# Kernel optimization log

Hardware: AMD Instinct MI355X
Metric: run time of the kernel (lower is better)

## Reference

```python
import jax, jax.numpy as jnp
import numpy as np
import math

E = 8          # num_exp
K = 2          # top-k
IN_D = 1024
HD = 2048
BS = 8
SEQ = 2048
CAP_FACTOR = 1.25
MIN_CAP = 4


def setup_inputs() -> dict:
    key = jax.random.key(0)
    ks = jax.random.split(key, 5)
    s = 0.02  # init scale for weights
    x = jax.random.normal(ks[0], (BS, SEQ, IN_D), jnp.float32)
    gate_w = jax.random.normal(ks[1], (E, IN_D), jnp.float32) * s
    fc1_w = jax.random.normal(ks[2], (E, HD, IN_D), jnp.float32) * s
    gating_w = jax.random.normal(ks[3], (E, HD, IN_D), jnp.float32) * s
    fc2_w = jax.random.normal(ks[4], (E, IN_D, HD), jnp.float32) * s
    return {"x": x, "gate_w": gate_w, "fc1_w": fc1_w, "gating_w": gating_w, "fc2_w": fc2_w}


def reference(x, gate_w, fc1_w, gating_w, fc2_w):
    bs, seq, d = x.shape
    N = bs * seq
    NK = N * K
    # capacity in slots per expert (static given shapes)
    capacity = max(int(math.ceil(((NK + E - 1) // E) * CAP_FACTOR)), MIN_CAP)
    dummy = E * capacity  # overflow slot index

    # --- routing ---
    logits = jnp.einsum('bsd,ed->bse', x, gate_w)
    probs = jax.nn.softmax(logits.astype(jnp.float32), axis=-1)
    # load-balancing probs use detached x
    logits_lbl = jnp.einsum('bsd,ed->bse', jax.lax.stop_gradient(x), gate_w)
    probs_lbl = jax.nn.softmax(logits_lbl.astype(jnp.float32), axis=-1)

    topk_vals, topk_inds = jax.lax.top_k(probs, K)          # [bs,seq,K]
    cl = topk_vals / (topk_vals.sum(-1, keepdims=True) + 1e-9)

    x_exp = jnp.repeat(x.reshape(N, d), K, axis=0)          # [NK, d]
    exp_ids = topk_inds.reshape(NK)
    w_flat = cl.reshape(NK).astype(x.dtype)

    # --- dispatch: stable sort by expert id ---
    sort_perm = jnp.argsort(exp_ids * NK + jnp.arange(NK))
    sorted_exp = exp_ids[sort_perm]
    sorted_x = x_exp[sort_perm]
    sorted_w = w_flat[sort_perm]

    counts = jnp.zeros((E,), jnp.int32).at[sorted_exp].add(1)
    starts = jnp.cumsum(counts) - counts
    local_pos = jnp.arange(NK) - starts[sorted_exp]
    keep = local_pos < capacity
    slot = jnp.where(keep, sorted_exp * capacity + local_pos, dummy)

    buf = jnp.zeros((dummy + 1, d), x.dtype).at[slot].set(sorted_x)
    buf_x = buf[:-1].reshape(E, capacity, d)

    # --- per-expert SwiGLU FFN as grouped matmuls ---
    h = jax.nn.silu(jnp.einsum('ecd,ehd->ech', buf_x, fc1_w)) * \
        jnp.einsum('ecd,ehd->ech', buf_x, gating_w)
    buf_out = jnp.einsum('ech,edh->ecd', h, fc2_w)           # [E,cap,d]

    # --- combine ---
    buf_full = jnp.concatenate([buf_out.reshape(dummy, d),
                                jnp.zeros((1, d), x.dtype)], axis=0)
    w_masked = sorted_w * keep.astype(sorted_w.dtype)
    out_sorted = buf_full[slot] * w_masked[:, None]
    out_dispatch = jnp.zeros((NK, d), x.dtype).at[sort_perm].set(out_sorted)
    moe_out = out_dispatch.reshape(N, K, d).sum(axis=1).reshape(bs, seq, d)

    # --- balancing loss ---
    p = probs_lbl.mean(axis=(0, 1))
    f = jax.lax.stop_gradient(
        jnp.zeros((E,), jnp.float32).at[exp_ids].add(1.0) / NK)
    balancing_loss = E * jnp.sum(p * f)
    return moe_out.astype(x.dtype), balancing_loss
```

## Files before the change

kernel.cpp:

```cpp
#include <hip/hip_runtime.h>

#define E_NUM 8
#define DIM   1024
#define HDIM  2048
#define N_TOK 16384
#define NKA   32768
#define CAP   5120
#define REG_SZ 16777216

typedef __bf16 bf16x8 __attribute__((ext_vector_type(8)));
typedef float  f32x4  __attribute__((ext_vector_type(4)));

__device__ __forceinline__ unsigned short f2b(float f) {
  union { float f; unsigned u; } v; v.f = f;
  unsigned r = (v.u + 0x7FFFu + ((v.u >> 16) & 1u)) >> 16;
  return (unsigned short)r;
}

__device__ __forceinline__ void gload16(const void* g, void* l) {
  __builtin_amdgcn_global_load_lds(
      (const __attribute__((address_space(1))) unsigned int*)g,
      (__attribute__((address_space(3))) unsigned int*)l, 16, 0, 0);
}

template<int N> __device__ __forceinline__ void wait_vmcnt() {
  if constexpr (N == 10)      asm volatile("s_waitcnt vmcnt(10)" ::: "memory");
  else if constexpr (N == 8)  asm volatile("s_waitcnt vmcnt(8)"  ::: "memory");
  else if constexpr (N == 4)  asm volatile("s_waitcnt vmcnt(4)"  ::: "memory");
  else if constexpr (N == 2)  asm volatile("s_waitcnt vmcnt(2)"  ::: "memory");
  else if constexpr (N == 0)  asm volatile("s_waitcnt vmcnt(0)"  ::: "memory");
}

__global__ __launch_bounds__(256) void cast_kernel(
    const float* __restrict__ s0, const float* __restrict__ s1,
    const float* __restrict__ s2, const float* __restrict__ s3,
    unsigned short* __restrict__ dst) {
  int region = blockIdx.y;
  const float* src = region == 0 ? s0 : region == 1 ? s1 : region == 2 ? s2 : s3;
  size_t i = ((size_t)blockIdx.x * 256 + threadIdx.x) * 8;
  float4 v0 = *(const float4*)(src + i);
  float4 v1 = *(const float4*)(src + i + 4);
  ushort4 u0 = { f2b(v0.x), f2b(v0.y), f2b(v0.z), f2b(v0.w) };
  ushort4 u1 = { f2b(v1.x), f2b(v1.y), f2b(v1.z), f2b(v1.w) };
  unsigned short* o = dst + (size_t)region * REG_SZ + i;
  *(ushort4*)o = u0;
  *(ushort4*)(o + 4) = u1;
}

__global__ __launch_bounds__(256) void routing_kernel(
    const float* __restrict__ x, const float* __restrict__ gate_w,
    int* __restrict__ cnt, float* __restrict__ p_sum,
    int* __restrict__ tok_of_slot, float* __restrict__ w_of_slot) {
  __shared__ float p_acc[E_NUM];
  __shared__ int   lcnt[E_NUM];
  __shared__ int   l_tok[E_NUM][128];
  __shared__ float l_w[E_NUM][128];
  __shared__ int   base[E_NUM];

  int t = threadIdx.x, lane = t & 63, wave = t >> 6;
  if (t < E_NUM) { p_acc[t] = 0.f; lcnt[t] = 0; }
  __syncthreads();

  for (int it = 0; it < 16; ++it) {
    int token = blockIdx.x * 64 + it * 4 + wave;
    const float4* xr = (const float4*)(x + (size_t)token * DIM);
    float4 xv[4];
    #pragma unroll
    for (int i = 0; i < 4; ++i) xv[i] = xr[lane + 64 * i];
    float s[E_NUM];
    #pragma unroll
    for (int e = 0; e < E_NUM; ++e) {
      const float4* gr = (const float4*)(gate_w + e * DIM);
      float acc = 0.f;
      #pragma unroll
      for (int i = 0; i < 4; ++i) {
        float4 g = gr[lane + 64 * i];
        acc += xv[i].x * g.x + xv[i].y * g.y + xv[i].z * g.z + xv[i].w * g.w;
      }
      s[e] = acc;
    }
    #pragma unroll
    for (int e = 0; e < E_NUM; ++e) {
      float v = s[e];
      #pragma unroll
      for (int off = 32; off; off >>= 1) v += __shfl_down(v, off);
      s[e] = v;
    }
    if (lane == 0) {
      float m = s[0];
      #pragma unroll
      for (int e = 1; e < E_NUM; ++e) m = fmaxf(m, s[e]);
      float p[E_NUM]; float sum = 0.f;
      #pragma unroll
      for (int e = 0; e < E_NUM; ++e) { p[e] = expf(s[e] - m); sum += p[e]; }
      float inv = 1.f / sum;
      #pragma unroll
      for (int e = 0; e < E_NUM; ++e) p[e] *= inv;
      int e0 = 0; float v0 = p[0];
      #pragma unroll
      for (int e = 1; e < E_NUM; ++e) if (p[e] > v0) { v0 = p[e]; e0 = e; }
      int e1 = -1; float v1 = -1.f;
      #pragma unroll
      for (int e = 0; e < E_NUM; ++e) if (e != e0 && p[e] > v1) { v1 = p[e]; e1 = e; }
      float denom = v0 + v1 + 1e-9f;
      float w0 = v0 / denom, w1 = v1 / denom;
      #pragma unroll
      for (int e = 0; e < E_NUM; ++e) atomicAdd(&p_acc[e], p[e]);
      int i0 = atomicAdd(&lcnt[e0], 1); l_tok[e0][i0] = token; l_w[e0][i0] = w0;
      int i1 = atomicAdd(&lcnt[e1], 1); l_tok[e1][i1] = token; l_w[e1][i1] = w1;
    }
  }
  __syncthreads();
  if (t < E_NUM) {
    base[t] = atomicAdd(&cnt[t], lcnt[t]);
    atomicAdd(&p_sum[t], p_acc[t]);
  }
  __syncthreads();
  int e = t >> 5, i0 = t & 31;
  int n = lcnt[e], b = base[e];
  for (int i = i0; i < n; i += 32) {
    int pos = b + i;
    if (pos < CAP) {
      tok_of_slot[e * CAP + pos] = l_tok[e][i];
      w_of_slot[e * CAP + pos]   = l_w[e][i];
    }
  }
}

__global__ void loss_kernel(const int* __restrict__ cnt,
                            const float* __restrict__ p_sum,
                            float* __restrict__ out_loss) {
  if (threadIdx.x == 0) {
    float acc = 0.f;
    for (int e = 0; e < E_NUM; ++e)
      acc += (p_sum[e] / (float)N_TOK) * ((float)cnt[e] / (float)NKA);
    *out_loss = (float)E_NUM * acc;
  }
}


__device__ __forceinline__ void lda_f(const unsigned short* Ab, bf16x8 af[2][4],
                                      int rowbase, const int cs[2]) {
  const unsigned short* base = Ab + rowbase * 64;
  #pragma unroll
  for (int mt = 0; mt < 4; ++mt) {
    af[0][mt] = *(const bf16x8*)&base[mt * 1024 + cs[0]];
    af[1][mt] = *(const bf16x8*)&base[mt * 1024 + cs[1]];
  }
}
__device__ __forceinline__ void ldb_f(const unsigned short* Bb, bf16x8 bf[2][2],
                                      int rowbase, const int cs[2]) {
  const unsigned short* base = Bb + rowbase * 64;
  #pragma unroll
  for (int nt = 0; nt < 2; ++nt) {
    bf[0][nt] = *(const bf16x8*)&base[nt * 1024 + cs[0]];
    bf[1][nt] = *(const bf16x8*)&base[nt * 1024 + cs[1]];
  }
}

template<int MH, int NH>
__device__ __forceinline__ void mmq(f32x4 acc[8][4], const bf16x8 af[2][4],
                                    const bf16x8 bf[2][2]) {
  #pragma unroll
  for (int mt = 0; mt < 4; ++mt)
    #pragma unroll
    for (int nt = 0; nt < 2; ++nt) {
      f32x4 c = acc[MH * 4 + mt][NH * 2 + nt];
      c = __builtin_amdgcn_mfma_f32_16x16x32_bf16(af[0][mt], bf[0][nt], c, 0, 0, 0);
      c = __builtin_amdgcn_mfma_f32_16x16x32_bf16(af[1][mt], bf[1][nt], c, 0, 0, 0);
      acc[MH * 4 + mt][NH * 2 + nt] = c;
    }
}

#define A_LDS(b) (&LDS[(b) * 16384])
#define B_LDS(b) (&LDS[32768 + (b) * 16384])

#define STAGE_A(b, h, kk) { \
  gload16(srcA[h][0] + (kk) * 64, &LDS[(b) * 16384 + (h) * 8192 + wave * 512]); \
  gload16(srcA[h][1] + (kk) * 64, &LDS[(b) * 16384 + (h) * 8192 + 4096 + wave * 512]); }
#define STAGE_B(b, h, kk) { \
  gload16(srcB[h][0] + (kk) * 64, &LDS[32768 + (b) * 16384 + (h) * 8192 + wave * 512]); \
  gload16(srcB[h][1] + (kk) * 64, &LDS[32768 + (b) * 16384 + (h) * 8192 + 4096 + wave * 512]); }

#define MIDBAR \
  __builtin_amdgcn_s_barrier(); \
  asm volatile("s_waitcnt lgkmcnt(0)" ::: "memory"); \
  __builtin_amdgcn_sched_barrier(0); \
  __builtin_amdgcn_s_setprio(1);

#define ENDBAR(W) \
  __builtin_amdgcn_s_setprio(0); \
  wait_vmcnt<W>(); \
  __builtin_amdgcn_s_barrier();

#define TILE_BODY(W1T, W2T, W4T, S1, S2) { \
  const int cur = kt & 1, oth = cur ^ 1; \
  lda_f(A_LDS(cur), af, g64r, cs); \
  ldb_f(B_LDS(cur), bfA, q32r, cs); \
  if (S1) STAGE_A(oth, 1, kt + 1); \
  MIDBAR; mmq<0, 0>(acc, af, bfA); ENDBAR(W1T); \
  ldb_f(B_LDS(cur), bfB, 128 + q32r, cs); \
  if (S2) STAGE_A(cur, 0, kt + 2); \
  MIDBAR; mmq<0, 1>(acc, af, bfB); ENDBAR(W2T); \
  lda_f(A_LDS(cur), af, 128 + g64r, cs); \
  if (S2) STAGE_B(cur, 0, kt + 2); \
  MIDBAR; mmq<1, 1>(acc, af, bfB); ENDBAR(-1); \
  if (S2) STAGE_B(cur, 1, kt + 2); \
  MIDBAR; mmq<1, 0>(acc, af, bfA); ENDBAR(W4T); \
}

#define GEMM_PROLOGUE { \
  STAGE_A(0, 0, 0); STAGE_B(0, 0, 0); STAGE_B(0, 1, 0); STAGE_A(0, 1, 0); \
  STAGE_A(1, 0, 1); STAGE_B(1, 0, 1); STAGE_B(1, 1, 1); \
  wait_vmcnt<10>(); \
  __builtin_amdgcn_s_barrier(); }

#define GEMM_MAIN(NTK) \
  GEMM_PROLOGUE; \
  for (int kt = 0; kt < (NTK) - 2; ++kt) TILE_BODY(10, 10, 10, true, true); \
  { int kt = (NTK) - 2; TILE_BODY(10, 8, 4, true, false); } \
  { int kt = (NTK) - 1; TILE_BODY(2, 0, -1, false, false); }

__global__ __launch_bounds__(512, 2) void gemm1_kernel(
    const unsigned short* __restrict__ Wb,
    const int* __restrict__ cnt, const int* __restrict__ tok_of_slot,
    unsigned short* __restrict__ Hbuf, int e_base) {
  int ez = blockIdx.z, e = e_base + ez;
  int cntc = min(cnt[e], CAP);
  int m0 = blockIdx.y * 256;
  if (m0 >= cntc) return;
  int n0 = blockIdx.x * 256;

  __shared__ __align__(16) unsigned short LDS[65536];

  int tid = threadIdx.x;
  int wave = tid >> 6, lane = tid & 63;
  int quad = lane >> 4, r = lane & 15;
  int gm = (wave >> 2) * 64, qn = (wave & 3) * 32;
  int g64r = gm + r, q32r = qn + r;
  int cs[2] = { (quad ^ (r & 7)) * 8, ((4 + quad) ^ (r & 7)) * 8 };

  const unsigned short* W1e = Wb + (size_t)e * HDIM * DIM;
  const unsigned short* Wge = Wb + REG_SZ + (size_t)e * HDIM * DIM;
  const unsigned short* Xb  = Wb + (size_t)3 * REG_SZ;

  const unsigned short* srcA[2][2];
  const unsigned short* srcB[2][2];
  #pragma unroll
  for (int j = 0; j < 2; ++j) {
    int row = (j * 512 + tid) >> 3;
    int co  = ((tid & 7) ^ (row & 7)) * 8;
    #pragma unroll
    for (int h = 0; h < 2; ++h) {
      int slot = m0 + h * 128 + row;
      int tok = (slot < cntc) ? tok_of_slot[e * CAP + slot] : 0;
      srcA[h][j] = Xb + (size_t)tok * DIM + co;
      int nglob = n0 + h * 128 + row;
      const unsigned short* wsrc = (nglob & 1) ? Wge : W1e;
      srcB[h][j] = wsrc + (size_t)(nglob >> 1) * DIM + co;
    }
  }

  f32x4 acc[8][4];
  #pragma unroll
  for (int i = 0; i < 8; ++i)
    #pragma unroll
    for (int jj = 0; jj < 4; ++jj) acc[i][jj] = (f32x4)0.f;
  bf16x8 af[2][4], bfA[2][2], bfB[2][2];

  GEMM_MAIN(16);

  #pragma unroll
  for (int mh = 0; mh < 2; ++mh)
    #pragma unroll
    for (int mt = 0; mt < 4; ++mt)
      #pragma unroll
      for (int reg = 0; reg < 4; ++reg) {
        int row = m0 + mh * 128 + gm + mt * 16 + quad * 4 + reg;
        bool wr = (row < cntc);
        size_t basei = (size_t)(ez * CAP + row) * HDIM;
        #pragma unroll
        for (int nh = 0; nh < 2; ++nh)
          #pragma unroll
          for (int nt = 0; nt < 2; ++nt) {
            float v = acc[mh * 4 + mt][nh * 2 + nt][reg];
            float o = __shfl_xor(v, 1);
            if (wr && !(lane & 1)) {
              float a = v, b = o;
              float hval = (a / (1.f + __expf(-a))) * b;
              int coln = n0 + nh * 128 + qn + nt * 16 + r;
              Hbuf[basei + (coln >> 1)] = f2b(hval);
            }
          }
      }
}

__global__ __launch_bounds__(512, 2) void gemm2_kernel(
    const unsigned short* __restrict__ Hbuf, const unsigned short* __restrict__ Wb,
    const int* __restrict__ cnt, const int* __restrict__ tok_of_slot,
    const float* __restrict__ w_of_slot, float* __restrict__ out, int e_base) {
  int ez = blockIdx.z, e = e_base + ez;
  int cntc = min(cnt[e], CAP);
  int m0 = blockIdx.y * 256;
  if (m0 >= cntc) return;
  int n0 = blockIdx.x * 256;

  __shared__ __align__(16) unsigned short LDS[65536];

  int tid = threadIdx.x;
  int wave = tid >> 6, lane = tid & 63;
  int quad = lane >> 4, r = lane & 15;
  int gm = (wave >> 2) * 64, qn = (wave & 3) * 32;
  int g64r = gm + r, q32r = qn + r;
  int cs[2] = { (quad ^ (r & 7)) * 8, ((4 + quad) ^ (r & 7)) * 8 };

  const unsigned short* W2e = Wb + (size_t)2 * REG_SZ + (size_t)e * DIM * HDIM;
  const unsigned short* He  = Hbuf + (size_t)(ez * CAP) * HDIM;

  const unsigned short* srcA[2][2];
  const unsigned short* srcB[2][2];
  #pragma unroll
  for (int j = 0; j < 2; ++j) {
    int row = (j * 512 + tid) >> 3;
    int co  = ((tid & 7) ^ (row & 7)) * 8;
    #pragma unroll
    for (int h = 0; h < 2; ++h) {
      srcA[h][j] = He + (size_t)(m0 + h * 128 + row) * HDIM + co;
      srcB[h][j] = W2e + (size_t)(n0 + h * 128 + row) * HDIM + co;
    }
  }

  f32x4 acc[8][4];
  #pragma unroll
  for (int i = 0; i < 8; ++i)
    #pragma unroll
    for (int jj = 0; jj < 4; ++jj) acc[i][jj] = (f32x4)0.f;
  bf16x8 af[2][4], bfA[2][2], bfB[2][2];

  GEMM_MAIN(32);

  #pragma unroll
  for (int mh = 0; mh < 2; ++mh)
    #pragma unroll
    for (int mt = 0; mt < 4; ++mt)
      #pragma unroll
      for (int reg = 0; reg < 4; ++reg) {
        int rowl = m0 + mh * 128 + gm + mt * 16 + quad * 4 + reg;
        if (rowl >= cntc) continue;
        int tok = tok_of_slot[e * CAP + rowl];
        float w = w_of_slot[e * CAP + rowl];
        float* orow = out + (size_t)tok * DIM + n0;
        #pragma unroll
        for (int nh = 0; nh < 2; ++nh)
          #pragma unroll
          for (int nt = 0; nt < 2; ++nt)
            atomicAdd(&orow[nh * 128 + qn + nt * 16 + r],
                      acc[mh * 4 + mt][nh * 2 + nt][reg] * w);
      }
}

extern "C" void kernel_launch(void* const* d_in, const int* in_sizes, int n_in,
                              void* d_out, int out_size, void* d_ws, size_t ws_size,
                              hipStream_t stream) {
  const float* x        = (const float*)d_in[0];
  const float* gate_w   = (const float*)d_in[1];
  const float* fc1_w    = (const float*)d_in[2];
  const float* gating_w = (const float*)d_in[3];
  const float* fc2_w    = (const float*)d_in[4];
  float* out = (float*)d_out;

  char* ws = (char*)d_ws;
  int*   cnt         = (int*)ws;
  float* p_sum       = (float*)(ws + 128);
  int*   tok_of_slot = (int*)(ws + 256);
  float* w_of_slot   = (float*)(ws + 256 + 163840);
  unsigned short* Wb   = (unsigned short*)(ws + 256 + 2 * 163840);
  size_t hbuf_off = 256 + 2 * 163840 + (size_t)4 * REG_SZ * 2;
  unsigned short* Hbuf = (unsigned short*)(ws + hbuf_off);

  const size_t per_e = (size_t)CAP * HDIM * 2;
  int chunkE = 1;
  if (ws_size > hbuf_off + per_e) {
    size_t c = (ws_size - hbuf_off) / per_e;
    chunkE = c >= 8 ? 8 : (int)c;
  }

  hipMemsetAsync(ws, 0, 256, stream);
  hipMemsetAsync(d_out, 0, (size_t)out_size * sizeof(float), stream);

  cast_kernel<<<dim3(8192, 4), 256, 0, stream>>>(fc1_w, gating_w, fc2_w, x, Wb);
  routing_kernel<<<256, 256, 0, stream>>>(x, gate_w, cnt, p_sum, tok_of_slot, w_of_slot);
  loss_kernel<<<1, 64, 0, stream>>>(cnt, p_sum, out + (size_t)N_TOK * DIM);

  for (int eb = 0; eb < E_NUM; eb += chunkE) {
    int ne = (E_NUM - eb) < chunkE ? (E_NUM - eb) : chunkE;
    gemm1_kernel<<<dim3(16, 20, ne), 512, 0, stream>>>(Wb, cnt, tok_of_slot, Hbuf, eb);
    gemm2_kernel<<<dim3(4, 20, ne), 512, 0, stream>>>(Hbuf, Wb, cnt, tok_of_slot, w_of_slot, out, eb);
  }
}
```

Baseline: 943.5 us.

## Replace atomic scatter with bf16 expert output buffer and gather-combine kernel

gemm2 no longer scatters its results into the fp32 output with atomicAdd. It writes bf16 per-slot rows into reused workspace regions (the dead fc1/gating weight copies and the x copy). A new combine kernel then gathers each token's two slots, weights them and writes the output, so the output memset and the atomic traffic go away. The x-to-bf16 cast is folded into the routing kernel, and blocks are remapped so that each XCD handles a single expert, which should improve L2 weight reuse. The cost is an extra bf16 rounding of the expert outputs and an extra kernel pass.

```diff
diff --git a/kernel.cpp b/kernel.cpp
--- a/kernel.cpp
+++ b/kernel.cpp
@@ -15,6 +15,11 @@
   union { float f; unsigned u; } v; v.f = f;
   unsigned r = (v.u + 0x7FFFu + ((v.u >> 16) & 1u)) >> 16;
   return (unsigned short)r;
+}
+
+__device__ __forceinline__ size_t obuf_off(int e) {
+  return (e < 6) ? (size_t)e * ((size_t)CAP * DIM)
+                 : (size_t)3 * REG_SZ + (size_t)(e - 6) * ((size_t)CAP * DIM);
 }
 
 __device__ __forceinline__ void gload16(const void* g, void* l) {
@@ -50,7 +55,9 @@
 __global__ __launch_bounds__(256) void routing_kernel(
     const float* __restrict__ x, const float* __restrict__ gate_w,
     int* __restrict__ cnt, float* __restrict__ p_sum,
-    int* __restrict__ tok_of_slot, float* __restrict__ w_of_slot) {
+    int* __restrict__ tok_of_slot, float* __restrict__ w_of_slot,
+    int* __restrict__ slot_of_tok, float* __restrict__ w_of_tok,
+    unsigned short* __restrict__ xb_out) {
   __shared__ float p_acc[E_NUM];
   __shared__ int   lcnt[E_NUM];
   __shared__ int   l_tok[E_NUM][128];
@@ -67,6 +74,12 @@
     float4 xv[4];
     #pragma unroll
     for (int i = 0; i < 4; ++i) xv[i] = xr[lane + 64 * i];
+    unsigned short* xo = xb_out + (size_t)token * DIM;
+    #pragma unroll
+    for (int i = 0; i < 4; ++i) {
+      ushort4 u = { f2b(xv[i].x), f2b(xv[i].y), f2b(xv[i].z), f2b(xv[i].w) };
+      *(ushort4*)(xo + 4 * (lane + 64 * i)) = u;
+    }
     float s[E_NUM];
     #pragma unroll
     for (int e = 0; e < E_NUM; ++e) {
@@ -106,8 +119,8 @@
       float w0 = v0 / denom, w1 = v1 / denom;
       #pragma unroll
       for (int e = 0; e < E_NUM; ++e) atomicAdd(&p_acc[e], p[e]);
-      int i0 = atomicAdd(&lcnt[e0], 1); l_tok[e0][i0] = token; l_w[e0][i0] = w0;
-      int i1 = atomicAdd(&lcnt[e1], 1); l_tok[e1][i1] = token; l_w[e1][i1] = w1;
+      int i0 = atomicAdd(&lcnt[e0], 1); l_tok[e0][i0] = (token << 1);     l_w[e0][i0] = w0;
+      int i1 = atomicAdd(&lcnt[e1], 1); l_tok[e1][i1] = (token << 1) | 1; l_w[e1][i1] = w1;
     }
   }
   __syncthreads();
@@ -121,8 +134,13 @@
   for (int i = i0; i < n; i += 32) {
     int pos = b + i;
     if (pos < CAP) {
-      tok_of_slot[e * CAP + pos] = l_tok[e][i];
-      w_of_slot[e * CAP + pos]   = l_w[e][i];
+      int tk = l_tok[e][i];
+      int token = tk >> 1, kb = tk & 1;
+      int slot = e * CAP + pos;
+      tok_of_slot[slot] = token;
+      w_of_slot[slot]   = l_w[e][i];
+      slot_of_tok[token * 2 + kb] = slot;
+      w_of_tok[token * 2 + kb]    = l_w[e][i];
     }
   }
 }
@@ -225,11 +243,21 @@
     const unsigned short* __restrict__ Wb,
     const int* __restrict__ cnt, const int* __restrict__ tok_of_slot,
     unsigned short* __restrict__ Hbuf, int e_base) {
-  int ez = blockIdx.z, e = e_base + ez;
+  int bx, by, bz;
+  if (gridDim.z == 8) {
+    int gid = blockIdx.x + (blockIdx.y << 4) + blockIdx.z * 320;
+    int xcd = gid & 7, j = gid >> 3;
+    int super = j >> 4, rem = j & 15;
+    bx = ((super & 3) << 2) + (rem & 3);
+    by = ((super >> 2) << 2) + (rem >> 2);
+    bz = xcd;
+  } else { bx = blockIdx.x; by = blockIdx.y; bz = blockIdx.z; }
+
+  int ez = bz, e = e_base + ez;
   int cntc = min(cnt[e], CAP);
-  int m0 = blockIdx.y * 256;
+  int m0 = by * 256;
   if (m0 >= cntc) return;
-  int n0 = blockIdx.x * 256;
+  int n0 = bx * 256;
 
   __shared__ __align__(16) unsigned short LDS[65536];
 
@@ -298,12 +326,23 @@
 __global__ __launch_bounds__(512, 2) void gemm2_kernel(
     const unsigned short* __restrict__ Hbuf, const unsigned short* __restrict__ Wb,
     const int* __restrict__ cnt, const int* __restrict__ tok_of_slot,
-    const float* __restrict__ w_of_slot, float* __restrict__ out, int e_base) {
-  int ez = blockIdx.z, e = e_base + ez;
+    const float* __restrict__ w_of_slot, float* __restrict__ out,
+    unsigned short* __restrict__ obuf, int use_obuf, int e_base) {
+  int bx, by, bz;
+  if (gridDim.z == 8) {
+    int gid = blockIdx.x + (blockIdx.y << 2) + blockIdx.z * 80;
+    int xcd = gid & 7, j = gid >> 3;
+    int super = j >> 4, rem = j & 15;
+    bx = rem & 3;
+    by = (super << 2) + (rem >> 2);
+    bz = xcd;
+  } else { bx = blockIdx.x; by = blockIdx.y; bz = blockIdx.z; }
+
+  int ez = bz, e = e_base + ez;
   int cntc = min(cnt[e], CAP);
-  int m0 = blockIdx.y * 256;
+  int m0 = by * 256;
   if (m0 >= cntc) return;
-  int n0 = blockIdx.x * 256;
+  int n0 = bx * 256;
 
   __shared__ __align__(16) unsigned short LDS[65536];
 
@@ -339,24 +378,86 @@
 
   GEMM_MAIN(32);
 
-  #pragma unroll
-  for (int mh = 0; mh < 2; ++mh)
-    #pragma unroll
-    for (int mt = 0; mt < 4; ++mt)
-      #pragma unroll
-      for (int reg = 0; reg < 4; ++reg) {
-        int rowl = m0 + mh * 128 + gm + mt * 16 + quad * 4 + reg;
-        if (rowl >= cntc) continue;
-        int tok = tok_of_slot[e * CAP + rowl];
-        float w = w_of_slot[e * CAP + rowl];
-        float* orow = out + (size_t)tok * DIM + n0;
+  if (use_obuf) {
+    size_t ob = obuf_off(e);
+    #pragma unroll
+    for (int mh = 0; mh < 2; ++mh)
+      #pragma unroll
+      for (int mt = 0; mt < 4; ++mt)
         #pragma unroll
-        for (int nh = 0; nh < 2; ++nh)
+        for (int reg = 0; reg < 4; ++reg) {
+          int rowl = m0 + mh * 128 + gm + mt * 16 + quad * 4 + reg;
+          bool wr = (rowl < cntc);
+          unsigned short* orow = obuf + ob + (size_t)rowl * DIM;
           #pragma unroll
-          for (int nt = 0; nt < 2; ++nt)
-            atomicAdd(&orow[nh * 128 + qn + nt * 16 + r],
-                      acc[mh * 4 + mt][nh * 2 + nt][reg] * w);
-      }
+          for (int nh = 0; nh < 2; ++nh)
+            #pragma unroll
+            for (int nt = 0; nt < 2; ++nt) {
+              float v = acc[mh * 4 + mt][nh * 2 + nt][reg];
+              float o = __shfl_xor(v, 1);
+              if (wr && !(lane & 1)) {
+                unsigned pack = (unsigned)f2b(v) | ((unsigned)f2b(o) << 16);
+                int col = n0 + nh * 128 + qn + nt * 16 + r;
+                *(unsigned*)(orow + col) = pack;
+              }
+            }
+        }
+  } else {
+    #pragma unroll
+    for (int mh = 0; mh < 2; ++mh)
+      #pragma unroll
+      for (int mt = 0; mt < 4; ++mt)
+        #pragma unroll
+        for (int reg = 0; reg < 4; ++reg) {
+          int rowl = m0 + mh * 128 + gm + mt * 16 + quad * 4 + reg;
+          if (rowl >= cntc) continue;
+          int tok = tok_of_slot[e * CAP + rowl];
+          float w = w_of_slot[e * CAP + rowl];
+          float* orow = out + (size_t)tok * DIM + n0;
+          #pragma unroll
+          for (int nh = 0; nh < 2; ++nh)
+            #pragma unroll
+            for (int nt = 0; nt < 2; ++nt)
+              atomicAdd(&orow[nh * 128 + qn + nt * 16 + r],
+                        acc[mh * 4 + mt][nh * 2 + nt][reg] * w);
+        }
+  }
+}
+
+__global__ __launch_bounds__(256) void combine_kernel(
+    const unsigned short* __restrict__ Wb,
+    const int* __restrict__ slot_of_tok, const float* __restrict__ w_of_tok,
+    float* __restrict__ out) {
+  int t = blockIdx.x * 256 + threadIdx.x;
+  int tok = t >> 6;
+  int d0 = (t & 63) * 16;
+  int s0 = slot_of_tok[2 * tok], s1 = slot_of_tok[2 * tok + 1];
+  float w0 = w_of_tok[2 * tok], w1 = w_of_tok[2 * tok + 1];
+
+  float acc[16];
+  #pragma unroll
+  for (int j = 0; j < 16; ++j) acc[j] = 0.f;
+
+  if (s0 >= 0) {
+    int e = s0 / CAP, pos = s0 % CAP;
+    const unsigned short* rp = Wb + obuf_off(e) + (size_t)pos * DIM + d0;
+    bf16x8 v0 = *(const bf16x8*)rp, v1 = *(const bf16x8*)(rp + 8);
+    #pragma unroll
+    for (int j = 0; j < 8; ++j) { acc[j] += w0 * (float)v0[j]; acc[8 + j] += w0 * (float)v1[j]; }
+  }
+  if (s1 >= 0) {
+    int e = s1 / CAP, pos = s1 % CAP;
+    const unsigned short* rp = Wb + obuf_off(e) + (size_t)pos * DIM + d0;
+    bf16x8 v0 = *(const bf16x8*)rp, v1 = *(const bf16x8*)(rp + 8);
+    #pragma unroll
+    for (int j = 0; j < 8; ++j) { acc[j] += w1 * (float)v0[j]; acc[8 + j] += w1 * (float)v1[j]; }
+  }
+  float* o = out + (size_t)tok * DIM + d0;
+  #pragma unroll
+  for (int q = 0; q < 4; ++q) {
+    float4 v = { acc[4 * q], acc[4 * q + 1], acc[4 * q + 2], acc[4 * q + 3] };
+    *(float4*)(o + 4 * q) = v;
+  }
 }
 
 extern "C" void kernel_launch(void* const* d_in, const int* in_sizes, int n_in,
@@ -374,8 +475,10 @@
   float* p_sum       = (float*)(ws + 128);
   int*   tok_of_slot = (int*)(ws + 256);
   float* w_of_slot   = (float*)(ws + 256 + 163840);
-  unsigned short* Wb   = (unsigned short*)(ws + 256 + 2 * 163840);
-  size_t hbuf_off = 256 + 2 * 163840 + (size_t)4 * REG_SZ * 2;
+  int*   slot_of_tok = (int*)(ws + 256 + 2 * 163840);
+  float* w_of_tok    = (float*)(ws + 256 + 2 * 163840 + 131072);
+  unsigned short* Wb = (unsigned short*)(ws + 256 + 2 * 163840 + 2 * 131072);
+  size_t hbuf_off = 256 + 2 * 163840 + 2 * 131072 + (size_t)4 * REG_SZ * 2;
   unsigned short* Hbuf = (unsigned short*)(ws + hbuf_off);
 
   const size_t per_e = (size_t)CAP * HDIM * 2;
@@ -384,17 +487,32 @@
     size_t c = (ws_size - hbuf_off) / per_e;
     chunkE = c >= 8 ? 8 : (int)c;
   }
+  int use_obuf = (chunkE == 8);
 
   hipMemsetAsync(ws, 0, 256, stream);
-  hipMemsetAsync(d_out, 0, (size_t)out_size * sizeof(float), stream);
-
-  cast_kernel<<<dim3(8192, 4), 256, 0, stream>>>(fc1_w, gating_w, fc2_w, x, Wb);
-  routing_kernel<<<256, 256, 0, stream>>>(x, gate_w, cnt, p_sum, tok_of_slot, w_of_slot);
+  if (use_obuf) {
+    hipMemsetAsync(slot_of_tok, 0xFF, 131072, stream);
+  } else {
+    hipMemsetAsync(d_out, 0, (size_t)out_size * sizeof(float), stream);
+  }
+
+  cast_kernel<<<dim3(8192, 3), 256, 0, stream>>>(fc1_w, gating_w, fc2_w, x, Wb);
+  routing_kernel<<<256, 256, 0, stream>>>(x, gate_w, cnt, p_sum, tok_of_slot,
+                                          w_of_slot, slot_of_tok, w_of_tok,
+                                          Wb + (size_t)3 * REG_SZ);
   loss_kernel<<<1, 64, 0, stream>>>(cnt, p_sum, out + (size_t)N_TOK * DIM);
 
-  for (int eb = 0; eb < E_NUM; eb += chunkE) {
-    int ne = (E_NUM - eb) < chunkE ? (E_NUM - eb) : chunkE;
-    gemm1_kernel<<<dim3(16, 20, ne), 512, 0, stream>>>(Wb, cnt, tok_of_slot, Hbuf, eb);
-    gemm2_kernel<<<dim3(4, 20, ne), 512, 0, stream>>>(Hbuf, Wb, cnt, tok_of_slot, w_of_slot, out, eb);
-  }
-}
+  if (use_obuf) {
+    gemm1_kernel<<<dim3(16, 20, 8), 512, 0, stream>>>(Wb, cnt, tok_of_slot, Hbuf, 0);
+    gemm2_kernel<<<dim3(4, 20, 8), 512, 0, stream>>>(Hbuf, Wb, cnt, tok_of_slot,
+                                                     w_of_slot, out, Wb, 1, 0);
+    combine_kernel<<<4096, 256, 0, stream>>>(Wb, slot_of_tok, w_of_tok, out);
+  } else {
+    for (int eb = 0; eb < E_NUM; eb += chunkE) {
+      int ne = (E_NUM - eb) < chunkE ? (E_NUM - eb) : chunkE;
+      gemm1_kernel<<<dim3(16, 20, ne), 512, 0, stream>>>(Wb, cnt, tok_of_slot, Hbuf, eb);
+      gemm2_kernel<<<dim3(4, 20, ne), 512, 0, stream>>>(Hbuf, Wb, cnt, tok_of_slot,
+                                                        w_of_slot, out, Wb, 0, eb);
+    }
+  }
+}
```

Measured after the change: 924.5 us. 1.02x faster.
